# Kernel tuning notes

Hardware: AMD Instinct MI355X
Metric: run time of the kernel (lower is better)

## Reference

```python
import jax, jax.numpy as jnp
import numpy as np

H = 3584        # hidden_size
NH = 16         # num_attention_heads
HD = 256        # head_dim
NKV = 8         # num_key_value_heads
GROUPS = NH // NKV
B, S = 2, 2048
SOFTCAP = 50.0
SCALE = 256.0 ** -0.5   # query_pre_attn_scalar ** -0.5
ROPE_BASE = 10000.0
NEG = -1e9


def _rotate_half(x):
    x1, x2 = jnp.split(x, 2, axis=-1)
    return jnp.concatenate([-x2, x1], axis=-1)


def _apply_rope(x, cos, sin):
    # x: [b, h, s, d]; cos/sin: [s, d]
    return x * cos[None, None] + _rotate_half(x) * sin[None, None]


def setup_inputs() -> dict:
    key = jax.random.key(0)
    k1, k2, k3, k4, k5 = jax.random.split(key, 5)
    hidden_states = jax.random.normal(k1, (B, S, H), dtype=jnp.float32)
    # additive causal mask [1, 1, S, S]
    causal = jnp.tril(jnp.ones((S, S), dtype=bool))
    attention_mask = jnp.where(causal, 0.0, NEG).astype(jnp.float32)[None, None]
    Wq = jax.random.normal(k2, (H, NH * HD), dtype=jnp.float32) * 0.02
    Wk = jax.random.normal(k3, (H, NKV * HD), dtype=jnp.float32) * 0.02
    Wv = jax.random.normal(k4, (H, NKV * HD), dtype=jnp.float32) * 0.02
    Wo = jax.random.normal(k5, (NH * HD, H), dtype=jnp.float32) * 0.02
    return {"hidden_states": hidden_states, "attention_mask": attention_mask,
            "Wq": Wq, "Wk": Wk, "Wv": Wv, "Wo": Wo}


def reference(hidden_states, attention_mask, Wq, Wk, Wv, Wo):
    b, s, _ = hidden_states.shape
    q = (hidden_states @ Wq).reshape(b, s, NH, HD).transpose(0, 2, 1, 3)   # [b,nh,s,d]
    k = (hidden_states @ Wk).reshape(b, s, NKV, HD).transpose(0, 2, 1, 3)  # [b,nkv,s,d]
    v = (hidden_states @ Wv).reshape(b, s, NKV, HD).transpose(0, 2, 1, 3)

    # RoPE (HF-style: freqs duplicated, rotate_half)
    pos = jnp.arange(s, dtype=jnp.float32)
    inv_freq = 1.0 / (ROPE_BASE ** (jnp.arange(0, HD, 2, dtype=jnp.float32) / HD))
    freqs = pos[:, None] * inv_freq[None, :]          # [s, d/2]
    emb = jnp.concatenate([freqs, freqs], axis=-1)    # [s, d]
    cos, sin = jnp.cos(emb), jnp.sin(emb)
    q = _apply_rope(q, cos, sin)
    k = _apply_rope(k, cos, sin)

    # repeat_kv for GQA
    k = jnp.repeat(k, GROUPS, axis=1)  # [b,nh,s,d]
    v = jnp.repeat(v, GROUPS, axis=1)

    scores = jnp.einsum('bhsd,bhtd->bhst', q, k) * SCALE
    # tanh logit softcapping
    scores = jnp.tanh(scores / SOFTCAP) * SOFTCAP
    scores = scores + attention_mask
    probs = jax.nn.softmax(scores.astype(jnp.float32), axis=-1).astype(q.dtype)
    out = jnp.einsum('bhst,bhtd->bhsd', probs, v)
    out = out.transpose(0, 2, 1, 3).reshape(b, s, NH * HD)
    return out @ Wo
```

## Files before the change

### kernel.cpp

```cpp
#include <hip/hip_runtime.h>
#include <cstdint>
#include <cstddef>

typedef __bf16 bf16x8 __attribute__((ext_vector_type(8)));
typedef float  f32x4  __attribute__((ext_vector_type(4)));
typedef unsigned short u16;

#define GLDS16(GP, LP) __builtin_amdgcn_global_load_lds( \
    (const __attribute__((address_space(1))) void*)(GP), \
    (__attribute__((address_space(3))) void*)(LP), 16, 0, 0)

__device__ __forceinline__ float b2f(u16 u) {
  unsigned int x = ((unsigned int)u) << 16;
  return __builtin_bit_cast(float, x);
}
__device__ __forceinline__ u16 f2b(float f) {
  unsigned int u = __builtin_bit_cast(unsigned int, f);
  unsigned int r = (u + 0x7fffu + ((u >> 16) & 1u)) >> 16;
  return (u16)r;
}

constexpr int Bc  = 2;
constexpr int Sc  = 2048;
constexpr int Hc  = 3584;
constexpr int NHc = 16;
constexpr int HDc = 256;
constexpr int NKV = 8;
constexpr int QD  = NHc * HDc;
constexpr int QS  = 8192;
constexpr float SCALE   = 0.0625f;
constexpr float CAP     = 50.0f;
constexpr float INV_CAP = 1.0f / 50.0f;

__device__ __forceinline__ float softcap(float raw) {
  float y = raw * (SCALE * INV_CAP);
  float a = __builtin_fabsf(y);
  float e = __expf(-2.0f * a);
  float t = (1.0f - e) * __builtin_amdgcn_rcpf(1.0f + e);
  return copysignf(t, y) * CAP;
}

__global__ void rope_table_k(float* __restrict__ cosT, float* __restrict__ sinT) {
  int idx = blockIdx.x * 256 + threadIdx.x;
  int s = idx >> 7, i = idx & 127;
  float inv = expf((float)i * -0.0719557841560639f);
  float ang = (float)s * inv;
  cosT[idx] = cosf(ang);
  sinT[idx] = sinf(ang);
}

__global__ void cvt_f32_bf16(const float4* __restrict__ in, ushort4* __restrict__ out, int n4) {
  int i = blockIdx.x * 256 + threadIdx.x;
  int st = gridDim.x * 256;
  for (; i < n4; i += st) {
    float4 v = in[i];
    ushort4 u;
    u.x = f2b(v.x); u.y = f2b(v.y); u.z = f2b(v.z); u.w = f2b(v.w);
    out[i] = u;
  }
}

__global__ void transpose_cvt(const float* __restrict__ in, u16* __restrict__ out, int R, int C) {
  __shared__ float t[32][33];
  int c0 = blockIdx.x * 32, r0 = blockIdx.y * 32;
  int tx = threadIdx.x, ty = threadIdx.y;
#pragma unroll
  for (int i = 0; i < 4; i++)
    t[ty + i * 8][tx] = in[(size_t)(r0 + ty + i * 8) * C + c0 + tx];
  __syncthreads();
#pragma unroll
  for (int i = 0; i < 4; i++)
    out[(size_t)(c0 + ty + i * 8) * R + r0 + tx] = f2b(t[tx][ty + i * 8]);
}

__global__ void transpose_v(const u16* __restrict__ QKV, u16* __restrict__ Vt) {
  __shared__ u16 t[32][33];
  int b = blockIdx.z >> 3, kvh = blockIdx.z & 7;
  int s0 = blockIdx.x * 32, d0 = blockIdx.y * 32;
  int tx = threadIdx.x, ty = threadIdx.y;
#pragma unroll
  for (int i = 0; i < 4; i++)
    t[ty + i * 8][tx] = QKV[(size_t)(b * Sc + s0 + ty + i * 8) * QS + 6144 + kvh * HDc + d0 + tx];
  __syncthreads();
#pragma unroll
  for (int i = 0; i < 4; i++)
    Vt[(size_t)((b * NKV + kvh) * HDc + d0 + ty + i * 8) * Sc + s0 + tx] = t[tx][ty + i * 8];
}

template <int NH>
__global__ void rope_apply(u16* __restrict__ X, const float* __restrict__ cosT,
                           const float* __restrict__ sinT) {
  constexpr int LS = (NH == 16) ? 4 : 3;
  int idx = blockIdx.x * 256 + threadIdx.x;
  const int i4 = (idx & 31) << 2;
  const int h = (idx >> 5) & (NH - 1);
  const int row = idx >> (5 + LS);
  const int s = row & (Sc - 1);
  u16* p = X + (size_t)row * QS + h * 256 + i4;
  ushort4 lo = *(const ushort4*)p;
  ushort4 hi = *(const ushort4*)(p + 128);
  float4 c = *(const float4*)(cosT + s * 128 + i4);
  float4 sn = *(const float4*)(sinT + s * 128 + i4);
  ushort4 nlo, nhi;
  { float xl = b2f(lo.x), xh = b2f(hi.x);
    nlo.x = f2b(xl * c.x - xh * sn.x); nhi.x = f2b(xh * c.x + xl * sn.x); }
  { float xl = b2f(lo.y), xh = b2f(hi.y);
    nlo.y = f2b(xl * c.y - xh * sn.y); nhi.y = f2b(xh * c.y + xl * sn.y); }
  { float xl = b2f(lo.z), xh = b2f(hi.z);
    nlo.z = f2b(xl * c.z - xh * sn.z); nhi.z = f2b(xh * c.z + xl * sn.z); }
  { float xl = b2f(lo.w), xh = b2f(hi.w);
    nlo.w = f2b(xl * c.w - xh * sn.w); nhi.w = f2b(xh * c.w + xl * sn.w); }
  *(ushort4*)p = nlo;
  *(ushort4*)(p + 128) = nhi;
}

template <typename OT>
__global__ __launch_bounds__(512, 1) void gemm256(const u16* __restrict__ A,
                                                  const u16* __restrict__ Bt,
                                                  OT* __restrict__ C,
                                                  int M, int N, int K, int GM) {
  __shared__ alignas(16) u16 As[2][256 * 64];
  __shared__ alignas(16) u16 Bs[2][256 * 64];
  const int nwg = gridDim.x;
  const int cpx = nwg >> 3;
  const int wgid = (blockIdx.x & 7) * cpx + (blockIdx.x >> 3);
  const int GN = nwg / GM;
  const int width = 8 * GN;
  const int grp = wgid / width;
  const int rem = wgid - grp * width;
  const int m0 = (grp * 8 + (rem & 7)) * 256;
  const int n0 = (rem >> 3) * 256;
  const int tid = threadIdx.x;
  const int lane = tid & 63;
  const int w = tid >> 6;
  const int wm = w >> 2, wn = w & 3;
  const int lg = lane >> 4, lr = lane & 15;
  const int nkt = K >> 6;

  auto STAGE = [&](int buf, int kt) {
    const int k0 = kt * 64;
#pragma unroll
    for (int i = 0; i < 4; i++) {
      int c = i * 512 + tid;
      int row = c >> 3, slot = c & 7;
      GLDS16(A + (size_t)(m0 + row) * K + k0 + (slot ^ (row & 7)) * 8,
             (char*)As[buf] + c * 16);
    }
#pragma unroll
    for (int i = 0; i < 4; i++) {
      int c = i * 512 + tid;
      int row = c >> 3, slot = c & 7;
      GLDS16(Bt + (size_t)(n0 + row) * K + k0 + (slot ^ (row & 7)) * 8,
             (char*)Bs[buf] + c * 16);
    }
  };

  f32x4 acc[8][4] = {};

  STAGE(0, 0);
  STAGE(1, 1);
  asm volatile("s_waitcnt vmcnt(8)" ::: "memory");
  __builtin_amdgcn_sched_barrier(0);
  __builtin_amdgcn_s_barrier();

  for (int kt = 0; kt < nkt; ++kt) {
    const int buf = kt & 1;
    bf16x8 bfr[4][2], af[4][2], af2[4][2];
#pragma unroll
    for (int j = 0; j < 4; j++)
#pragma unroll
      for (int ks = 0; ks < 2; ks++) {
        int row = wn * 64 + j * 16 + lr;
        int sl = (ks * 4 + lg) ^ (row & 7);
        bfr[j][ks] = *(const bf16x8*)&Bs[buf][row * 64 + sl * 8];
      }
#pragma unroll
    for (int i = 0; i < 4; i++)
#pragma unroll
      for (int ks = 0; ks < 2; ks++) {
        int row = wm * 128 + i * 16 + lr;
        int sl = (ks * 4 + lg) ^ (row & 7);
        af[i][ks] = *(const bf16x8*)&As[buf][row * 64 + sl * 8];
      }
#pragma unroll
    for (int i = 0; i < 4; i++)
#pragma unroll
      for (int ks = 0; ks < 2; ks++) {
        int row = wm * 128 + 64 + i * 16 + lr;
        int sl = (ks * 4 + lg) ^ (row & 7);
        af2[i][ks] = *(const bf16x8*)&As[buf][row * 64 + sl * 8];
      }
    __builtin_amdgcn_s_setprio(1);
#pragma unroll
    for (int i = 0; i < 4; i++)
#pragma unroll
      for (int j = 0; j < 4; j++)
#pragma unroll
        for (int ks = 0; ks < 2; ks++)
          acc[i][j] = __builtin_amdgcn_mfma_f32_16x16x32_bf16(
              af[i][ks], bfr[j][ks], acc[i][j], 0, 0, 0);
    __builtin_amdgcn_s_setprio(0);
    asm volatile("s_waitcnt vmcnt(0) lgkmcnt(0)" ::: "memory");
    __builtin_amdgcn_sched_barrier(0);
    __builtin_amdgcn_s_barrier();
    if (kt + 2 < nkt) STAGE(buf, kt + 2);
    __builtin_amdgcn_s_setprio(1);
#pragma unroll
    for (int i = 0; i < 4; i++)
#pragma unroll
      for (int j = 0; j < 4; j++)
#pragma unroll
        for (int ks = 0; ks < 2; ks++)
          acc[4 + i][j] = __builtin_amdgcn_mfma_f32_16x16x32_bf16(
              af2[i][ks], bfr[j][ks], acc[4 + i][j], 0, 0, 0);
    __builtin_amdgcn_s_setprio(0);
  }

#pragma unroll
  for (int i = 0; i < 8; i++) {
    const int row = m0 + wm * 128 + i * 16 + lg * 4;
#pragma unroll
    for (int j = 0; j < 4; j++) {
      const int col = n0 + wn * 64 + j * 16 + lr;
#pragma unroll
      for (int r = 0; r < 4; r++) {
        if constexpr (sizeof(OT) == 2)
          C[(size_t)(row + r) * N + col] = f2b(acc[i][j][r]);
        else
          C[(size_t)(row + r) * N + col] = acc[i][j][r];
      }
    }
  }
}

__global__ __launch_bounds__(512, 1) void attn_fwd(const u16* __restrict__ QKV,
                                                   const u16* __restrict__ Vt,
                                                   u16* __restrict__ AO) {
  constexpr int KVB = 64;
  __shared__ alignas(16) u16 Ks[2][KVB * 256];
  __shared__ alignas(16) u16 Vs[2][256 * KVB];
  __shared__ alignas(16) u16 Ps[8][16][72];
  const int bx = blockIdx.x, h = blockIdx.y, b = blockIdx.z;
  const int qt = b ? (15 - bx) : bx;
  const int q0 = qt * 128;
  const int kvh = h >> 1;
  const int tid = threadIdx.x, w = tid >> 6, lane = tid & 63;
  const int lg = lane >> 4, lr = lane & 15;

  bf16x8 qf[8];
  {
    const u16* qp = QKV + (size_t)(b * Sc + q0 + w * 16 + lr) * QS + h * HDc + lg * 8;
#pragma unroll
    for (int kk = 0; kk < 8; kk++) qf[kk] = *(const bf16x8*)(qp + kk * 32);
  }

  f32x4 o[16] = {};
  float m_r[4], l_r[4];
#pragma unroll
  for (int r = 0; r < 4; r++) { m_r[r] = -1e30f; l_r[r] = 0.0f; }
  const int my_qrow = q0 + w * 16 + lg * 4;
  const int wave_min_row = q0 + w * 16;
  const int wave_max_row = q0 + w * 16 + 15;

  const u16* kbase = QKV + (size_t)(b * Sc) * QS + 4096 + kvh * HDc;
  const u16* vbase = Vt + (size_t)((b * NKV + kvh) * HDc) * Sc;

  auto STAGE = [&](int buf, int t0) {
#pragma unroll
    for (int i = 0; i < 4; i++) {
      int c = i * 512 + tid;
      int row = c >> 5, slot = c & 31;
      int gs = slot ^ (row & 7);
      GLDS16(kbase + (size_t)(t0 + row) * QS + gs * 8, (char*)Ks[buf] + c * 16);
    }
#pragma unroll
    for (int i = 0; i < 4; i++) {
      int c = i * 512 + tid;
      int d = c >> 3, slot = c & 7;
      int gs = slot ^ (d & 7);
      GLDS16(vbase + (size_t)d * Sc + t0 + gs * 8, (char*)Vs[buf] + c * 16);
    }
  };

  const int nt = 2 * qt + 2;
  int cur = 0;
  STAGE(0, 0);
  for (int ti = 0; ti < nt; ++ti) {
    const int t0 = ti * 64;
    if (ti + 1 < nt) {
      STAGE(cur ^ 1, t0 + 64);
      asm volatile("s_waitcnt vmcnt(8)" ::: "memory");
    } else {
      asm volatile("s_waitcnt vmcnt(0)" ::: "memory");
    }
    __builtin_amdgcn_sched_barrier(0);
    __builtin_amdgcn_s_barrier();

    if (t0 <= wave_max_row) {
      const u16* KsT = Ks[cur];
      const u16* VsT = Vs[cur];

      f32x4 sc[4];
#pragma unroll
      for (int j = 0; j < 4; j++) {
        f32x4 a = {0.f, 0.f, 0.f, 0.f};
        const int row = j * 16 + lr;
#pragma unroll
        for (int kk = 0; kk < 8; kk++) {
          int s0 = (kk * 4 + lg) ^ (lr & 7);
          bf16x8 kf = *(const bf16x8*)&KsT[row * 256 + s0 * 8];
          a = __builtin_amdgcn_mfma_f32_16x16x32_bf16(qf[kk], kf, a, 0, 0, 0);
        }
        sc[j] = a;
      }

      float tmax[4] = {-1e30f, -1e30f, -1e30f, -1e30f};
      if (t0 + 63 > wave_min_row) {
#pragma unroll
        for (int j = 0; j < 4; j++)
#pragma unroll
          for (int r = 0; r < 4; r++) {
            float x = softcap(sc[j][r]);
            if (t0 + j * 16 + lr > my_qrow + r) x = -1e9f;
            sc[j][r] = x;
            tmax[r] = fmaxf(tmax[r], x);
          }
      } else {
#pragma unroll
        for (int j = 0; j < 4; j++)
#pragma unroll
          for (int r = 0; r < 4; r++) {
            float x = softcap(sc[j][r]);
            sc[j][r] = x;
            tmax[r] = fmaxf(tmax[r], x);
          }
      }
#pragma unroll
      for (int xm = 1; xm < 16; xm <<= 1)
#pragma unroll
        for (int r = 0; r < 4; r++) tmax[r] = fmaxf(tmax[r], __shfl_xor(tmax[r], xm, 64));

      bool need = false;
#pragma unroll
      for (int r = 0; r < 4; r++) need |= (tmax[r] > m_r[r] + 8.0f);
      if (__any(need)) {
        float scal[4];
#pragma unroll
        for (int r = 0; r < 4; r++) {
          float mn = fmaxf(m_r[r], tmax[r]);
          scal[r] = __expf(m_r[r] - mn);
          m_r[r] = mn;
          l_r[r] *= scal[r];
        }
#pragma unroll
        for (int df = 0; df < 16; df++)
#pragma unroll
          for (int r = 0; r < 4; r++) o[df][r] *= scal[r];
      }

      float psum[4] = {0.f, 0.f, 0.f, 0.f};
#pragma unroll
      for (int j = 0; j < 4; j++)
#pragma unroll
        for (int r = 0; r < 4; r++) {
          float p = __expf(sc[j][r] - m_r[r]);
          psum[r] += p;
          Ps[w][lg * 4 + r][j * 16 + lr] = f2b(p);
        }
#pragma unroll
      for (int xm = 1; xm < 16; xm <<= 1)
#pragma unroll
        for (int r = 0; r < 4; r++) psum[r] += __shfl_xor(psum[r], xm, 64);
#pragma unroll
      for (int r = 0; r < 4; r++) l_r[r] += psum[r];

      bf16x8 pf0 = *(const bf16x8*)&Ps[w][lr][lg * 8];
      bf16x8 pf1 = *(const bf16x8*)&Ps[w][lr][32 + lg * 8];
#pragma unroll
      for (int df = 0; df < 16; df++) {
        const int d = df * 16 + lr;
        int s0 = lg ^ (lr & 7);
        int s1 = (4 + lg) ^ (lr & 7);
        bf16x8 vf0 = *(const bf16x8*)&VsT[d * KVB + s0 * 8];
        o[df] = __builtin_amdgcn_mfma_f32_16x16x32_bf16(pf0, vf0, o[df], 0, 0, 0);
        bf16x8 vf1 = *(const bf16x8*)&VsT[d * KVB + s1 * 8];
        o[df] = __builtin_amdgcn_mfma_f32_16x16x32_bf16(pf1, vf1, o[df], 0, 0, 0);
      }
    }

    __builtin_amdgcn_s_barrier();
    cur ^= 1;
  }

  float inv_l[4];
#pragma unroll
  for (int r = 0; r < 4; r++) inv_l[r] = 1.0f / l_r[r];
  u16* op = AO + (size_t)(b * Sc + my_qrow) * QD + h * HDc + lr;
#pragma unroll
  for (int df = 0; df < 16; df++)
#pragma unroll
    for (int r = 0; r < 4; r++)
      op[(size_t)r * QD + df * 16] = f2b(o[df][r] * inv_l[r]);
}

extern "C" void kernel_launch(void* const* d_in, const int* in_sizes, int n_in,
                              void* d_out, int out_size, void* d_ws, size_t ws_size,
                              hipStream_t stream) {
  (void)in_sizes; (void)n_in; (void)out_size; (void)ws_size;
  const float* hs = (const float*)d_in[0];
  const float* Wq = (const float*)d_in[2];
  const float* Wk = (const float*)d_in[3];
  const float* Wv = (const float*)d_in[4];
  const float* Wo = (const float*)d_in[5];
  float* out = (float*)d_out;
  char* ws = (char*)d_ws;

  float* cosT = (float*)(ws + 0);
  float* sinT = (float*)(ws + 1048576);
  u16* hsb    = (u16*)(ws + 2097152);
  u16* Wqkvt  = (u16*)(ws + 31457280);
  u16* Wot    = (u16*)(ws + 90177536);
  u16* QKVb   = (u16*)(ws + 119537664);
  u16* Vtr    = hsb;
  u16* AO     = Wqkvt;

  dim3 tb32x8(32, 8);

  rope_table_k<<<1024, 256, 0, stream>>>(cosT, sinT);
  cvt_f32_bf16<<<2048, 256, 0, stream>>>((const float4*)hs, (ushort4*)hsb, (Bc * Sc * Hc) / 4);
  transpose_cvt<<<dim3(QD / 32, Hc / 32), tb32x8, 0, stream>>>(Wq, Wqkvt, Hc, QD);
  transpose_cvt<<<dim3(2048 / 32, Hc / 32), tb32x8, 0, stream>>>(Wk, Wqkvt + (size_t)4096 * Hc, Hc, 2048);
  transpose_cvt<<<dim3(2048 / 32, Hc / 32), tb32x8, 0, stream>>>(Wv, Wqkvt + (size_t)6144 * Hc, Hc, 2048);
  transpose_cvt<<<dim3(Hc / 32, QD / 32), tb32x8, 0, stream>>>(Wo, Wot, QD, Hc);

  gemm256<u16><<<dim3(16 * 32), 512, 0, stream>>>(hsb, Wqkvt, QKVb, Bc * Sc, QS, Hc, 16);

  rope_apply<16><<<8192, 256, 0, stream>>>(QKVb, cosT, sinT);
  rope_apply<8><<<4096, 256, 0, stream>>>(QKVb + 4096, cosT, sinT);
  transpose_v<<<dim3(Sc / 32, HDc / 32, Bc * NKV), tb32x8, 0, stream>>>(QKVb, Vtr);

  attn_fwd<<<dim3(16, NHc, Bc), 512, 0, stream>>>(QKVb, Vtr, AO);

  gemm256<float><<<dim3(16 * 14), 512, 0, stream>>>(AO, Wot, out, Bc * Sc, Hc, QD, 16);
}
```

Baseline: 611.4 us.

## Fuse Q RoPE into attention and halve KV tile to 32

The separate RoPE kernel for Q is removed, and each attention wave now applies rotary embedding to its Q fragment in registers after loading it. The attention KV tile shrinks from 64 to 32 rows, and the launch bound drops the one-block-per-CU hint. The smaller LDS footprint is meant to let more blocks share a CU. The trade-off is twice as many loop iterations, barriers and softmax reductions per query tile. A few GEMM index expressions are also inlined, which is cosmetic.

Result: slower. 666.8 us (+9.1%).

```diff
diff --git a/kernel.cpp b/kernel.cpp
--- a/kernel.cpp
+++ b/kernel.cpp
@@ -3,6 +3,7 @@
 #include <cstddef>
 
 typedef __bf16 bf16x8 __attribute__((ext_vector_type(8)));
+typedef unsigned short u16x8 __attribute__((ext_vector_type(8)));
 typedef float  f32x4  __attribute__((ext_vector_type(4)));
 typedef unsigned short u16;
 
@@ -171,24 +172,21 @@
 #pragma unroll
       for (int ks = 0; ks < 2; ks++) {
         int row = wn * 64 + j * 16 + lr;
-        int sl = (ks * 4 + lg) ^ (row & 7);
-        bfr[j][ks] = *(const bf16x8*)&Bs[buf][row * 64 + sl * 8];
+        bfr[j][ks] = *(const bf16x8*)&Bs[buf][row * 64 + ((ks * 4 + lg) ^ (row & 7)) * 8];
       }
 #pragma unroll
     for (int i = 0; i < 4; i++)
 #pragma unroll
       for (int ks = 0; ks < 2; ks++) {
         int row = wm * 128 + i * 16 + lr;
-        int sl = (ks * 4 + lg) ^ (row & 7);
-        af[i][ks] = *(const bf16x8*)&As[buf][row * 64 + sl * 8];
+        af[i][ks] = *(const bf16x8*)&As[buf][row * 64 + ((ks * 4 + lg) ^ (row & 7)) * 8];
       }
 #pragma unroll
     for (int i = 0; i < 4; i++)
 #pragma unroll
       for (int ks = 0; ks < 2; ks++) {
         int row = wm * 128 + 64 + i * 16 + lr;
-        int sl = (ks * 4 + lg) ^ (row & 7);
-        af2[i][ks] = *(const bf16x8*)&As[buf][row * 64 + sl * 8];
+        af2[i][ks] = *(const bf16x8*)&As[buf][row * 64 + ((ks * 4 + lg) ^ (row & 7)) * 8];
       }
     __builtin_amdgcn_s_setprio(1);
 #pragma unroll
@@ -233,26 +231,49 @@
   }
 }
 
-__global__ __launch_bounds__(512, 1) void attn_fwd(const u16* __restrict__ QKV,
-                                                   const u16* __restrict__ Vt,
-                                                   u16* __restrict__ AO) {
-  constexpr int KVB = 64;
+__global__ __launch_bounds__(512) void attn_fwd(const u16* __restrict__ QKV,
+                                                const u16* __restrict__ Vt,
+                                                const float* __restrict__ cosT,
+                                                const float* __restrict__ sinT,
+                                                u16* __restrict__ AO) {
+  constexpr int KVB = 32;
   __shared__ alignas(16) u16 Ks[2][KVB * 256];
   __shared__ alignas(16) u16 Vs[2][256 * KVB];
-  __shared__ alignas(16) u16 Ps[8][16][72];
+  __shared__ alignas(16) u16 Ps[8][16][40];
   const int bx = blockIdx.x, h = blockIdx.y, b = blockIdx.z;
   const int qt = b ? (15 - bx) : bx;
   const int q0 = qt * 128;
   const int kvh = h >> 1;
   const int tid = threadIdx.x, w = tid >> 6, lane = tid & 63;
   const int lg = lane >> 4, lr = lane & 15;
-
+  const int myrow = q0 + w * 16 + lr;
+
+  u16x8 qr[8];
+  {
+    const u16* qp = QKV + (size_t)(b * Sc + myrow) * QS + h * HDc + lg * 8;
+#pragma unroll
+    for (int kk = 0; kk < 8; kk++) qr[kk] = *(const u16x8*)(qp + kk * 32);
+    const float* ct = cosT + myrow * 128 + lg * 8;
+    const float* st = sinT + myrow * 128 + lg * 8;
+#pragma unroll
+    for (int kk = 0; kk < 4; kk++)
+#pragma unroll
+      for (int q4 = 0; q4 < 2; q4++) {
+        float4 c = *(const float4*)(ct + kk * 32 + q4 * 4);
+        float4 s = *(const float4*)(st + kk * 32 + q4 * 4);
+#pragma unroll
+        for (int e = 0; e < 4; e++) {
+          int ei = q4 * 4 + e;
+          float cc = (&c.x)[e], ss = (&s.x)[e];
+          float lo = b2f(qr[kk][ei]), hi = b2f(qr[kk + 4][ei]);
+          qr[kk][ei]     = f2b(lo * cc - hi * ss);
+          qr[kk + 4][ei] = f2b(hi * cc + lo * ss);
+        }
+      }
+  }
   bf16x8 qf[8];
-  {
-    const u16* qp = QKV + (size_t)(b * Sc + q0 + w * 16 + lr) * QS + h * HDc + lg * 8;
-#pragma unroll
-    for (int kk = 0; kk < 8; kk++) qf[kk] = *(const bf16x8*)(qp + kk * 32);
-  }
+#pragma unroll
+  for (int kk = 0; kk < 8; kk++) qf[kk] = __builtin_bit_cast(bf16x8, qr[kk]);
 
   f32x4 o[16] = {};
   float m_r[4], l_r[4];
@@ -267,29 +288,29 @@
 
   auto STAGE = [&](int buf, int t0) {
 #pragma unroll
-    for (int i = 0; i < 4; i++) {
+    for (int i = 0; i < 2; i++) {
       int c = i * 512 + tid;
       int row = c >> 5, slot = c & 31;
-      int gs = slot ^ (row & 7);
-      GLDS16(kbase + (size_t)(t0 + row) * QS + gs * 8, (char*)Ks[buf] + c * 16);
-    }
-#pragma unroll
-    for (int i = 0; i < 4; i++) {
+      GLDS16(kbase + (size_t)(t0 + row) * QS + (slot ^ (row & 7)) * 8,
+             (char*)Ks[buf] + c * 16);
+    }
+#pragma unroll
+    for (int i = 0; i < 2; i++) {
       int c = i * 512 + tid;
-      int d = c >> 3, slot = c & 7;
-      int gs = slot ^ (d & 7);
-      GLDS16(vbase + (size_t)d * Sc + t0 + gs * 8, (char*)Vs[buf] + c * 16);
+      int d = c >> 2, slot = c & 3;
+      GLDS16(vbase + (size_t)d * Sc + t0 + (slot ^ (d & 3)) * 8,
+             (char*)Vs[buf] + c * 16);
     }
   };
 
-  const int nt = 2 * qt + 2;
+  const int nt = 4 * qt + 4;
   int cur = 0;
   STAGE(0, 0);
   for (int ti = 0; ti < nt; ++ti) {
-    const int t0 = ti * 64;
+    const int t0 = ti * 32;
     if (ti + 1 < nt) {
-      STAGE(cur ^ 1, t0 + 64);
-      asm volatile("s_waitcnt vmcnt(8)" ::: "memory");
+      STAGE(cur ^ 1, t0 + 32);
+      asm volatile("s_waitcnt vmcnt(4)" ::: "memory");
     } else {
       asm volatile("s_waitcnt vmcnt(0)" ::: "memory");
     }
@@ -300,9 +321,9 @@
       const u16* KsT = Ks[cur];
       const u16* VsT = Vs[cur];
 
-      f32x4 sc[4];
-#pragma unroll
-      for (int j = 0; j < 4; j++) {
+      f32x4 sc[2];
+#pragma unroll
+      for (int j = 0; j < 2; j++) {
         f32x4 a = {0.f, 0.f, 0.f, 0.f};
         const int row = j * 16 + lr;
 #pragma unroll
@@ -315,9 +336,9 @@
       }
 
       float tmax[4] = {-1e30f, -1e30f, -1e30f, -1e30f};
-      if (t0 + 63 > wave_min_row) {
-#pragma unroll
-        for (int j = 0; j < 4; j++)
+      if (t0 + 31 > wave_min_row) {
+#pragma unroll
+        for (int j = 0; j < 2; j++)
 #pragma unroll
           for (int r = 0; r < 4; r++) {
             float x = softcap(sc[j][r]);
@@ -327,7 +348,7 @@
           }
       } else {
 #pragma unroll
-        for (int j = 0; j < 4; j++)
+        for (int j = 0; j < 2; j++)
 #pragma unroll
           for (int r = 0; r < 4; r++) {
             float x = softcap(sc[j][r]);
@@ -360,7 +381,7 @@
 
       float psum[4] = {0.f, 0.f, 0.f, 0.f};
 #pragma unroll
-      for (int j = 0; j < 4; j++)
+      for (int j = 0; j < 2; j++)
 #pragma unroll
         for (int r = 0; r < 4; r++) {
           float p = __expf(sc[j][r] - m_r[r]);
@@ -374,17 +395,13 @@
 #pragma unroll
       for (int r = 0; r < 4; r++) l_r[r] += psum[r];
 
-      bf16x8 pf0 = *(const bf16x8*)&Ps[w][lr][lg * 8];
-      bf16x8 pf1 = *(const bf16x8*)&Ps[w][lr][32 + lg * 8];
+      bf16x8 pf = *(const bf16x8*)&Ps[w][lr][lg * 8];
 #pragma unroll
       for (int df = 0; df < 16; df++) {
         const int d = df * 16 + lr;
-        int s0 = lg ^ (lr & 7);
-        int s1 = (4 + lg) ^ (lr & 7);
-        bf16x8 vf0 = *(const bf16x8*)&VsT[d * KVB + s0 * 8];
-        o[df] = __builtin_amdgcn_mfma_f32_16x16x32_bf16(pf0, vf0, o[df], 0, 0, 0);
-        bf16x8 vf1 = *(const bf16x8*)&VsT[d * KVB + s1 * 8];
-        o[df] = __builtin_amdgcn_mfma_f32_16x16x32_bf16(pf1, vf1, o[df], 0, 0, 0);
+        int s0 = lg ^ (d & 3);
+        bf16x8 vf = *(const bf16x8*)&VsT[d * KVB + s0 * 8];
+        o[df] = __builtin_amdgcn_mfma_f32_16x16x32_bf16(pf, vf, o[df], 0, 0, 0);
       }
     }
 
@@ -435,11 +452,10 @@
 
   gemm256<u16><<<dim3(16 * 32), 512, 0, stream>>>(hsb, Wqkvt, QKVb, Bc * Sc, QS, Hc, 16);
 
-  rope_apply<16><<<8192, 256, 0, stream>>>(QKVb, cosT, sinT);
   rope_apply<8><<<4096, 256, 0, stream>>>(QKVb + 4096, cosT, sinT);
   transpose_v<<<dim3(Sc / 32, HDc / 32, Bc * NKV), tb32x8, 0, stream>>>(QKVb, Vtr);
 
-  attn_fwd<<<dim3(16, NHc, Bc), 512, 0, stream>>>(QKVb, Vtr, AO);
+  attn_fwd<<<dim3(16, NHc, Bc), 512, 0, stream>>>(QKVb, Vtr, cosT, sinT, AO);
 
   gemm256<float><<<dim3(16 * 14), 512, 0, stream>>>(AO, Wot, out, Bc * Sc, Hc, QD, 16);
 }
```
